# Performance work log

Measured on AMD Instinct MI355X. Metric: run time of the kernel, lower is better.

## Reference

```python
import jax, jax.numpy as jnp
import numpy as np
import math

NUM_HEADS = 8
EMB = 256

def setup_inputs() -> dict:
    key = jax.random.key(0)
    ks = jax.random.split(key, 9)
    B_, N, C = 1024, 64, EMB  # 16 images * 64 windows, 8x8 window, C=256
    nW = 64
    q = jax.random.normal(ks[0], (B_, N, C), dtype=jnp.float32)
    k = jax.random.normal(ks[1], (B_, N, C), dtype=jnp.float32)
    v = jax.random.normal(ks[2], (B_, N, C), dtype=jnp.float32)
    mask = jax.random.normal(ks[3], (nW, N, N), dtype=jnp.float32)
    # MLP params (Linear: y = x @ W^T + b; we store W already transposed for x @ W)
    hid = 4 * C
    s1 = 1.0 / math.sqrt(C)
    s2 = 1.0 / math.sqrt(hid)
    w1 = jax.random.uniform(ks[4], (C, hid), minval=-s1, maxval=s1, dtype=jnp.float32)
    b1 = jax.random.uniform(ks[5], (hid,), minval=-s1, maxval=s1, dtype=jnp.float32)
    w2 = jax.random.uniform(ks[6], (hid, C), minval=-s2, maxval=s2, dtype=jnp.float32)
    b2 = jax.random.uniform(ks[7], (C,), minval=-s2, maxval=s2, dtype=jnp.float32)
    return {"q": q, "k": k, "v": v, "mask": mask, "H": 64, "W": 64,
            "w1": w1, "b1": b1, "w2": w2, "b2": b2}

def reference(q, k, v, mask, H, W, w1, b1, w2, b2):
    B_, N, C = q.shape
    h = NUM_HEADS
    d = C // h
    # separate heads: (B_, h, N, d)
    qh = q.reshape(B_, N, h, d).transpose(0, 2, 1, 3)
    kh = k.reshape(B_, N, h, d).transpose(0, 2, 1, 3)
    vh = v.reshape(B_, N, h, d).transpose(0, 2, 1, 3)
    attn = jnp.einsum('bhnd,bhmd->bhnm', qh, kh)  # raw scores
    nW = mask.shape[0]
    # additive window mask BEFORE scaling (faithful to original order)
    attn = attn.reshape(B_ // nW, nW, h, N, N) + mask[None, :, None, :, :]
    attn = attn.reshape(B_, h, N, N) / math.sqrt(d)
    attn = jax.nn.softmax(attn, axis=-1)
    out = jnp.einsum('bhnm,bhmd->bhnd', attn, vh)
    out = out.transpose(0, 2, 1, 3).reshape(B_, N, C)  # recombine heads
    # linear Mlp (dropout is identity at p=0.0); torch nn.GELU is exact erf
    hmid = jax.nn.gelu(out @ w1 + b1, approximate=False)
    out = out + (hmid @ w2 + b2)
    return out
```

## Files before the change

### kernel.cpp

```cpp
#include <hip/hip_runtime.h>
#include <hip/hip_bf16.h>
#include <cstdint>
#include <cstddef>

typedef __attribute__((ext_vector_type(8))) short bf16x8;
typedef __attribute__((ext_vector_type(4))) float f32x4;

static __device__ __forceinline__ unsigned short f2bf(float f) {
    __hip_bfloat16 h = __float2bfloat16(f);
    return *reinterpret_cast<unsigned short*>(&h);
}

static __device__ __forceinline__ f32x4 mfma_bf16(bf16x8 a, bf16x8 b, f32x4 c) {
    return __builtin_amdgcn_mfma_f32_16x16x32_bf16(a, b, c, 0, 0, 0);
}

static __device__ __forceinline__ bf16x8 pack8(float4 a, float4 b) {
    bf16x8 f;
    f[0]=(short)f2bf(a.x); f[1]=(short)f2bf(a.y); f[2]=(short)f2bf(a.z); f[3]=(short)f2bf(a.w);
    f[4]=(short)f2bf(b.x); f[5]=(short)f2bf(b.y); f[6]=(short)f2bf(b.z); f[7]=(short)f2bf(b.w);
    return f;
}

static __device__ __forceinline__ float gelu_erf(float v) {
    float s = v * 0.70710678118654752f;
    float a = fabsf(s);
    float t = __builtin_amdgcn_rcpf(1.0f + 0.3275911f * a);
    float poly = ((((1.061405429f * t - 1.453152027f) * t + 1.421413741f) * t
                   - 0.284496736f) * t + 0.254829592f) * t;
    float e = 1.0f - poly * __expf(-a * a);
    float erfv = copysignf(e, s);
    return 0.5f * v * (1.0f + erfv);
}

static __device__ __forceinline__ void load_lds16(const unsigned short* g, unsigned short* l) {
    __builtin_amdgcn_global_load_lds(
        (const __attribute__((address_space(1))) unsigned int*)g,
        (__attribute__((address_space(3))) unsigned int*)l, 16, 0, 0);
}

__global__ __launch_bounds__(256) void attn_kernel(
    const float* __restrict__ q, const float* __restrict__ k,
    const float* __restrict__ v, const float* __restrict__ mask,
    float* __restrict__ xout)
{
    __shared__ unsigned short Qs[64][40];
    __shared__ unsigned short Ks[64][40];
    __shared__ unsigned short Vt[32][72];
    __shared__ unsigned short Ps[64][72];

    const int tid  = threadIdx.x;
    const int b    = blockIdx.x >> 3;
    const int h    = blockIdx.x & 7;
    const int lane = tid & 63;
    const int l15  = lane & 15;
    const int g    = lane >> 4;
    const int w    = tid >> 6;

    {
        int row = tid >> 2;
        int seg = tid & 3;
        size_t base = ((size_t)(b * 64 + row)) * 256 + h * 32 + seg * 8;

        float4 a0 = *(const float4*)(q + base);
        float4 a1 = *(const float4*)(q + base + 4);
        unsigned short* p = &Qs[row][seg * 8];
        p[0]=f2bf(a0.x); p[1]=f2bf(a0.y); p[2]=f2bf(a0.z); p[3]=f2bf(a0.w);
        p[4]=f2bf(a1.x); p[5]=f2bf(a1.y); p[6]=f2bf(a1.z); p[7]=f2bf(a1.w);

        a0 = *(const float4*)(k + base);
        a1 = *(const float4*)(k + base + 4);
        p = &Ks[row][seg * 8];
        p[0]=f2bf(a0.x); p[1]=f2bf(a0.y); p[2]=f2bf(a0.z); p[3]=f2bf(a0.w);
        p[4]=f2bf(a1.x); p[5]=f2bf(a1.y); p[6]=f2bf(a1.z); p[7]=f2bf(a1.w);

        a0 = *(const float4*)(v + base);
        a1 = *(const float4*)(v + base + 4);
        int c = seg * 8;
        Vt[c + 0][row] = f2bf(a0.x);
        Vt[c + 1][row] = f2bf(a0.y);
        Vt[c + 2][row] = f2bf(a0.z);
        Vt[c + 3][row] = f2bf(a0.w);
        Vt[c + 4][row] = f2bf(a1.x);
        Vt[c + 5][row] = f2bf(a1.y);
        Vt[c + 6][row] = f2bf(a1.z);
        Vt[c + 7][row] = f2bf(a1.w);
    }
    __syncthreads();

    f32x4 s[4];
    {
        bf16x8 aQ = *(const bf16x8*)&Qs[w * 16 + l15][g * 8];
        #pragma unroll
        for (int ct = 0; ct < 4; ++ct) {
            bf16x8 bK = *(const bf16x8*)&Ks[ct * 16 + l15][g * 8];
            f32x4 z = {0.f, 0.f, 0.f, 0.f};
            s[ct] = mfma_bf16(aQ, bK, z);
        }
    }

    const float* mbase = mask + (size_t)(b & 63) * 4096;
    const float INV = 0.17677669529663688f;
    float rsum[4];
    #pragma unroll
    for (int r = 0; r < 4; ++r) {
        int row = w * 16 + g * 4 + r;
        float pr[4];
        #pragma unroll
        for (int ct = 0; ct < 4; ++ct)
            pr[ct] = (s[ct][r] + mbase[row * 64 + ct * 16 + l15]) * INV;
        float m = fmaxf(fmaxf(pr[0], pr[1]), fmaxf(pr[2], pr[3]));
        #pragma unroll
        for (int off = 1; off < 16; off <<= 1)
            m = fmaxf(m, __shfl_xor(m, off));
        float sum = 0.f;
        #pragma unroll
        for (int ct = 0; ct < 4; ++ct) { pr[ct] = __expf(pr[ct] - m); sum += pr[ct]; }
        #pragma unroll
        for (int off = 1; off < 16; off <<= 1)
            sum += __shfl_xor(sum, off);
        rsum[r] = sum;
        #pragma unroll
        for (int ct = 0; ct < 4; ++ct)
            Ps[row][ct * 16 + l15] = f2bf(pr[ct]);
    }

    f32x4 o[2] = {};
    #pragma unroll
    for (int ks = 0; ks < 2; ++ks) {
        bf16x8 pa = *(const bf16x8*)&Ps[w * 16 + l15][ks * 32 + g * 8];
        #pragma unroll
        for (int n = 0; n < 2; ++n) {
            bf16x8 vb = *(const bf16x8*)&Vt[n * 16 + l15][ks * 32 + g * 8];
            o[n] = mfma_bf16(pa, vb, o[n]);
        }
    }

    #pragma unroll
    for (int n = 0; n < 2; ++n) {
        #pragma unroll
        for (int r = 0; r < 4; ++r) {
            int row = w * 16 + g * 4 + r;
            xout[((size_t)(b * 64 + row)) * 256 + h * 32 + n * 16 + l15] =
                o[n][r] / rsum[r];
        }
    }
}

__global__ __launch_bounds__(256) void prep_w1(const float* __restrict__ src,
                                               unsigned short* __restrict__ dst)
{
    __shared__ float tile[64][65];
    const int kt = blockIdx.x, nb = blockIdx.y;
    const int t = threadIdx.x;
    const int r0 = t >> 4, c4 = (t & 15) * 4;
    #pragma unroll
    for (int p = 0; p < 4; ++p) {
        int kk = r0 + p * 16;
        float4 d = *(const float4*)(src + (size_t)(kt * 64 + kk) * 1024 + nb * 64 + c4);
        tile[kk][c4+0]=d.x; tile[kk][c4+1]=d.y; tile[kk][c4+2]=d.z; tile[kk][c4+3]=d.w;
    }
    __syncthreads();
    #pragma unroll
    for (int i = 0; i < 2; ++i) {
        int f = t + 256 * i;
        int chalf = f >> 8;
        int ksl   = (f >> 7) & 1;
        int nt    = (f >> 6) & 1;
        int gv    = (f >> 4) & 3;
        int l15v  = f & 15;
        int n_local = chalf * 32 + 8 * (l15v >> 2) + 4 * nt + (l15v & 3);
        int k_local = ksl * 32 + gv * 8;
        int c  = nb * 2 + chalf;
        int ks = kt * 2 + ksl;
        unsigned short tmp[8];
        #pragma unroll
        for (int e = 0; e < 8; ++e) tmp[e] = f2bf(tile[k_local + e][n_local]);
        size_t off = (size_t)c * 8192 + (size_t)((ks * 2 + nt) * 512)
                   + (gv * 16 + l15v) * 8;
        *(bf16x8*)(dst + off) = *(const bf16x8*)tmp;
    }
}

__global__ __launch_bounds__(256) void prep_w2(const float* __restrict__ src,
                                               unsigned short* __restrict__ dst)
{
    __shared__ float tile[64][65];
    const int ob = blockIdx.x, kb = blockIdx.y;
    const int t = threadIdx.x;
    const int r0 = t >> 4, c4 = (t & 15) * 4;
    #pragma unroll
    for (int p = 0; p < 4; ++p) {
        int kk = r0 + p * 16;
        float4 d = *(const float4*)(src + (size_t)(kb * 64 + kk) * 256 + ob * 64 + c4);
        tile[kk][c4+0]=d.x; tile[kk][c4+1]=d.y; tile[kk][c4+2]=d.z; tile[kk][c4+3]=d.w;
    }
    __syncthreads();
    #pragma unroll
    for (int i = 0; i < 2; ++i) {
        int f = t + 256 * i;
        int ksl = f >> 8;
        int tq  = (f >> 6) & 3;
        int gv  = (f >> 4) & 3;
        int l15v = f & 15;
        int c_local = tq * 16 + l15v;
        int k_local = ksl * 32 + gv * 8;
        int c = kb * 2 + ksl;
        unsigned short tmp[8];
        #pragma unroll
        for (int e = 0; e < 8; ++e) tmp[e] = f2bf(tile[k_local + e][c_local]);
        size_t off = (size_t)c * 8192 + (size_t)((ob * 4 + tq) * 512)
                   + (gv * 16 + l15v) * 8;
        *(bf16x8*)(dst + off) = *(const bf16x8*)tmp;
    }
}

__global__ __launch_bounds__(512, 4) void mlp_fused(
    const float* __restrict__ xin, float* __restrict__ xio,
    const unsigned short* __restrict__ wt1, const float* __restrict__ b1,
    const unsigned short* __restrict__ wt2, const float* __restrict__ b2)
{
    __shared__ unsigned short w1c[2][8192];
    __shared__ unsigned short w2c[2][8192];
    __shared__ float b1s[1024];

    const int tid  = threadIdx.x;
    const int lane = tid & 63;
    const int l15  = lane & 15;
    const int g    = lane >> 4;
    const int wid  = tid >> 6;
    const int fb   = (g * 16 + l15) * 8;

    const size_t rowbase = (size_t)blockIdx.x * 128;

    auto stage = [&](const unsigned short* gbase, unsigned short* lbase) {
        #pragma unroll
        for (int i = 0; i < 2; ++i) {
            load_lds16(gbase + (i * 512 + tid) * 8,
                       lbase + (i * 512 + wid * 64) * 8);
        }
    };

    stage(wt1, &w1c[0][0]);
    stage(wt2, &w2c[0][0]);

    b1s[tid]       = b1[tid];
    b1s[tid + 512] = b1[tid + 512];

    bf16x8 xf[8];
    {
        const float* xr = xin + (rowbase + wid * 16 + l15) * 256;
        #pragma unroll
        for (int ks = 0; ks < 8; ++ks) {
            float4 a0 = *(const float4*)(xr + ks * 32 + g * 8);
            float4 a1 = *(const float4*)(xr + ks * 32 + g * 8 + 4);
            xf[ks] = pack8(a0, a1);
        }
    }

    f32x4 oacc[16] = {};

    for (int hc = 0; hc < 32; ++hc) {
        const int cur = hc & 1;
        __syncthreads();

        if (hc < 31) {
            stage(wt1 + (size_t)(hc + 1) * 8192, &w1c[cur ^ 1][0]);
            stage(wt2 + (size_t)(hc + 1) * 8192, &w2c[cur ^ 1][0]);
        }

        f32x4 hacc[2] = {};
        #pragma unroll
        for (int ks = 0; ks < 8; ++ks) {
            bf16x8 w0 = *(const bf16x8*)&w1c[cur][(ks * 2 + 0) * 512 + fb];
            bf16x8 w1f = *(const bf16x8*)&w1c[cur][(ks * 2 + 1) * 512 + fb];
            hacc[0] = mfma_bf16(w0,  xf[ks], hacc[0]);
            hacc[1] = mfma_bf16(w1f, xf[ks], hacc[1]);
        }

        const float* bp = &b1s[hc * 32 + g * 8];
        float4 ba = *(const float4*)bp;
        float4 bb = *(const float4*)(bp + 4);
        bf16x8 aH;
        aH[0] = (short)f2bf(gelu_erf(hacc[0][0] + ba.x));
        aH[1] = (short)f2bf(gelu_erf(hacc[0][1] + ba.y));
        aH[2] = (short)f2bf(gelu_erf(hacc[0][2] + ba.z));
        aH[3] = (short)f2bf(gelu_erf(hacc[0][3] + ba.w));
        aH[4] = (short)f2bf(gelu_erf(hacc[1][0] + bb.x));
        aH[5] = (short)f2bf(gelu_erf(hacc[1][1] + bb.y));
        aH[6] = (short)f2bf(gelu_erf(hacc[1][2] + bb.z));
        aH[7] = (short)f2bf(gelu_erf(hacc[1][3] + bb.w));

        #pragma unroll
        for (int n = 0; n < 16; ++n) {
            bf16x8 bF = *(const bf16x8*)&w2c[cur][n * 512 + fb];
            oacc[n] = mfma_bf16(aH, bF, oacc[n]);
        }
    }

    #pragma unroll
    for (int n = 0; n < 16; ++n) {
        int col = n * 16 + l15;
        float bias = b2[col];
        #pragma unroll
        for (int r = 0; r < 4; ++r) {
            size_t idx = (rowbase + wid * 16 + g * 4 + r) * 256 + col;
            xio[idx] = oacc[n][r] + bias + xio[idx];
        }
    }
}

extern "C" void kernel_launch(void* const* d_in, const int* in_sizes, int n_in,
                              void* d_out, int out_size, void* d_ws, size_t ws_size,
                              hipStream_t stream)
{
    const float* q    = (const float*)d_in[0];
    const float* k    = (const float*)d_in[1];
    const float* v    = (const float*)d_in[2];
    const float* mask = (const float*)d_in[3];
    const float* w1   = (const float*)d_in[6];
    const float* b1   = (const float*)d_in[7];
    const float* w2   = (const float*)d_in[8];
    const float* b2   = (const float*)d_in[9];

    float* xio = (float*)d_out;

    unsigned short* wt1 = (unsigned short*)d_ws;
    unsigned short* wt2 = wt1 + (size_t)1024 * 256;

    prep_w1<<<dim3(4, 16), 256, 0, stream>>>(w1, wt1);
    prep_w2<<<dim3(4, 16), 256, 0, stream>>>(w2, wt2);

    attn_kernel<<<8192, 256, 0, stream>>>(q, k, v, mask, xio);

    mlp_fused<<<512, 512, 0, stream>>>(xio, xio, wt1, b1, wt2, b2);
}
```

Baseline: 170.0 us.

## Process two 16-row tiles per wave in fused MLP to halve weight streaming

Each wave now handles 32 rows instead of 16, so every staged W1/W2 chunk in LDS and each LDS fragment read feeds twice as many MFMAs. The grid drops from 512 to 256 blocks, which halves the total global weight traffic and LDS reads per output. In exchange, accumulator registers double (32 f32x4 oacc), launch bounds are relaxed to 2 blocks per CU, and 256 blocks may underfill the device's CUs.

```diff
diff --git a/kernel.cpp b/kernel.cpp
--- a/kernel.cpp
+++ b/kernel.cpp
@@ -215,7 +215,7 @@
     }
 }
 
-__global__ __launch_bounds__(512, 4) void mlp_fused(
+__global__ __launch_bounds__(512, 2) void mlp_fused(
     const float* __restrict__ xin, float* __restrict__ xio,
     const unsigned short* __restrict__ wt1, const float* __restrict__ b1,
     const unsigned short* __restrict__ wt2, const float* __restrict__ b2)
@@ -231,7 +231,7 @@
     const int wid  = tid >> 6;
     const int fb   = (g * 16 + l15) * 8;
 
-    const size_t rowbase = (size_t)blockIdx.x * 128;
+    const size_t rowbase = (size_t)blockIdx.x * 256;
 
     auto stage = [&](const unsigned short* gbase, unsigned short* lbase) {
         #pragma unroll
@@ -247,18 +247,19 @@
     b1s[tid]       = b1[tid];
     b1s[tid + 512] = b1[tid + 512];
 
-    bf16x8 xf[8];
-    {
-        const float* xr = xin + (rowbase + wid * 16 + l15) * 256;
+    bf16x8 xf[2][8];
+    #pragma unroll
+    for (int mt = 0; mt < 2; ++mt) {
+        const float* xr = xin + (rowbase + wid * 32 + mt * 16 + l15) * 256;
         #pragma unroll
         for (int ks = 0; ks < 8; ++ks) {
             float4 a0 = *(const float4*)(xr + ks * 32 + g * 8);
             float4 a1 = *(const float4*)(xr + ks * 32 + g * 8 + 4);
-            xf[ks] = pack8(a0, a1);
-        }
-    }
-
-    f32x4 oacc[16] = {};
+            xf[mt][ks] = pack8(a0, a1);
+        }
+    }
+
+    f32x4 oacc[2][16] = {};
 
     for (int hc = 0; hc < 32; ++hc) {
         const int cur = hc & 1;
@@ -269,43 +270,52 @@
             stage(wt2 + (size_t)(hc + 1) * 8192, &w2c[cur ^ 1][0]);
         }
 
-        f32x4 hacc[2] = {};
+        f32x4 hacc[2][2] = {};
         #pragma unroll
         for (int ks = 0; ks < 8; ++ks) {
-            bf16x8 w0 = *(const bf16x8*)&w1c[cur][(ks * 2 + 0) * 512 + fb];
+            bf16x8 w0  = *(const bf16x8*)&w1c[cur][(ks * 2 + 0) * 512 + fb];
             bf16x8 w1f = *(const bf16x8*)&w1c[cur][(ks * 2 + 1) * 512 + fb];
-            hacc[0] = mfma_bf16(w0,  xf[ks], hacc[0]);
-            hacc[1] = mfma_bf16(w1f, xf[ks], hacc[1]);
+            hacc[0][0] = mfma_bf16(w0,  xf[0][ks], hacc[0][0]);
+            hacc[0][1] = mfma_bf16(w1f, xf[0][ks], hacc[0][1]);
+            hacc[1][0] = mfma_bf16(w0,  xf[1][ks], hacc[1][0]);
+            hacc[1][1] = mfma_bf16(w1f, xf[1][ks], hacc[1][1]);
         }
 
         const float* bp = &b1s[hc * 32 + g * 8];
         float4 ba = *(const float4*)bp;
         float4 bb = *(const float4*)(bp + 4);
-        bf16x8 aH;
-        aH[0] = (short)f2bf(gelu_erf(hacc[0][0] + ba.x));
-        aH[1] = (short)f2bf(gelu_erf(hacc[0][1] + ba.y));
-        aH[2] = (short)f2bf(gelu_erf(hacc[0][2] + ba.z));
-        aH[3] = (short)f2bf(gelu_erf(hacc[0][3] + ba.w));
-        aH[4] = (short)f2bf(gelu_erf(hacc[1][0] + bb.x));
-        aH[5] = (short)f2bf(gelu_erf(hacc[1][1] + bb.y));
-        aH[6] = (short)f2bf(gelu_erf(hacc[1][2] + bb.z));
-        aH[7] = (short)f2bf(gelu_erf(hacc[1][3] + bb.w));
+        bf16x8 aH[2];
+        #pragma unroll
+        for (int mt = 0; mt < 2; ++mt) {
+            aH[mt][0] = (short)f2bf(gelu_erf(hacc[mt][0][0] + ba.x));
+            aH[mt][1] = (short)f2bf(gelu_erf(hacc[mt][0][1] + ba.y));
+            aH[mt][2] = (short)f2bf(gelu_erf(hacc[mt][0][2] + ba.z));
+            aH[mt][3] = (short)f2bf(gelu_erf(hacc[mt][0][3] + ba.w));
+            aH[mt][4] = (short)f2bf(gelu_erf(hacc[mt][1][0] + bb.x));
+            aH[mt][5] = (short)f2bf(gelu_erf(hacc[mt][1][1] + bb.y));
+            aH[mt][6] = (short)f2bf(gelu_erf(hacc[mt][1][2] + bb.z));
+            aH[mt][7] = (short)f2bf(gelu_erf(hacc[mt][1][3] + bb.w));
+        }
 
         #pragma unroll
         for (int n = 0; n < 16; ++n) {
             bf16x8 bF = *(const bf16x8*)&w2c[cur][n * 512 + fb];
-            oacc[n] = mfma_bf16(aH, bF, oacc[n]);
-        }
-    }
-
-    #pragma unroll
-    for (int n = 0; n < 16; ++n) {
-        int col = n * 16 + l15;
-        float bias = b2[col];
-        #pragma unroll
-        for (int r = 0; r < 4; ++r) {
-            size_t idx = (rowbase + wid * 16 + g * 4 + r) * 256 + col;
-            xio[idx] = oacc[n][r] + bias + xio[idx];
+            oacc[0][n] = mfma_bf16(aH[0], bF, oacc[0][n]);
+            oacc[1][n] = mfma_bf16(aH[1], bF, oacc[1][n]);
+        }
+    }
+
+    #pragma unroll
+    for (int mt = 0; mt < 2; ++mt) {
+        #pragma unroll
+        for (int n = 0; n < 16; ++n) {
+            int col = n * 16 + l15;
+            float bias = b2[col];
+            #pragma unroll
+            for (int r = 0; r < 4; ++r) {
+                size_t idx = (rowbase + wid * 32 + mt * 16 + g * 4 + r) * 256 + col;
+                xio[idx] = oacc[mt][n][r] + bias + xio[idx];
+            }
         }
     }
 }
@@ -333,5 +343,5 @@
 
     attn_kernel<<<8192, 256, 0, stream>>>(q, k, v, mask, xio);
 
-    mlp_fused<<<512, 512, 0, stream>>>(xio, xio, wt1, b1, wt2, b2);
-}
+    mlp_fused<<<256, 512, 0, stream>>>(xio, xio, wt1, b1, wt2, b2);
+}
```

Result: slower. 175.2 us (+3.1%).

## Software-pipeline MLP so next chunk's GEMM1+GELU overlaps current GEMM2

Applied to the files above, without the earlier changes.

Restructures the hidden-chunk loop. The first-layer matmul and erf-GELU for chunk i+1 are now computed while the second-layer MFMAs for chunk i run, so the independent VALU work can interleave with matrix instructions. The first-layer weights are prefetched two chunks ahead and the second-layer weights one chunk ahead, using the existing double buffers. The cost is higher register pressure from carrying aH alongside aH_next, plus one redundant first-layer/GELU computation on the final iteration.

```diff
diff --git a/kernel.cpp b/kernel.cpp
--- a/kernel.cpp
+++ b/kernel.cpp
@@ -241,8 +241,9 @@
         }
     };
 
-    stage(wt1, &w1c[0][0]);
-    stage(wt2, &w2c[0][0]);
+    stage(wt1,        &w1c[0][0]);
+    stage(wt2,        &w2c[0][0]);
+    stage(wt1 + 8192, &w1c[1][0]);
 
     b1s[tid]       = b1[tid];
     b1s[tid + 512] = b1[tid + 512];
@@ -260,28 +261,21 @@
 
     f32x4 oacc[16] = {};
 
-    for (int hc = 0; hc < 32; ++hc) {
-        const int cur = hc & 1;
-        __syncthreads();
-
-        if (hc < 31) {
-            stage(wt1 + (size_t)(hc + 1) * 8192, &w1c[cur ^ 1][0]);
-            stage(wt2 + (size_t)(hc + 1) * 8192, &w2c[cur ^ 1][0]);
-        }
-
+    __syncthreads();
+
+    bf16x8 aH;
+    {
         f32x4 hacc[2] = {};
         #pragma unroll
         for (int ks = 0; ks < 8; ++ks) {
-            bf16x8 w0 = *(const bf16x8*)&w1c[cur][(ks * 2 + 0) * 512 + fb];
-            bf16x8 w1f = *(const bf16x8*)&w1c[cur][(ks * 2 + 1) * 512 + fb];
+            bf16x8 w0  = *(const bf16x8*)&w1c[0][(ks * 2 + 0) * 512 + fb];
+            bf16x8 w1f = *(const bf16x8*)&w1c[0][(ks * 2 + 1) * 512 + fb];
             hacc[0] = mfma_bf16(w0,  xf[ks], hacc[0]);
             hacc[1] = mfma_bf16(w1f, xf[ks], hacc[1]);
         }
-
-        const float* bp = &b1s[hc * 32 + g * 8];
+        const float* bp = &b1s[g * 8];
         float4 ba = *(const float4*)bp;
         float4 bb = *(const float4*)(bp + 4);
-        bf16x8 aH;
         aH[0] = (short)f2bf(gelu_erf(hacc[0][0] + ba.x));
         aH[1] = (short)f2bf(gelu_erf(hacc[0][1] + ba.y));
         aH[2] = (short)f2bf(gelu_erf(hacc[0][2] + ba.z));
@@ -290,12 +284,48 @@
         aH[5] = (short)f2bf(gelu_erf(hacc[1][1] + bb.y));
         aH[6] = (short)f2bf(gelu_erf(hacc[1][2] + bb.z));
         aH[7] = (short)f2bf(gelu_erf(hacc[1][3] + bb.w));
-
+    }
+
+    for (int i = 0; i < 32; ++i) {
+        __syncthreads();
+
+        if (i < 31) {
+            stage(wt2 + (size_t)(i + 1) * 8192, &w2c[(i + 1) & 1][0]);
+            if (i < 30)
+                stage(wt1 + (size_t)(i + 2) * 8192, &w1c[i & 1][0]);
+        }
+
+        f32x4 hacc[2] = {};
+        const unsigned short* w1b = &w1c[(i + 1) & 1][0];
+        #pragma unroll
+        for (int ks = 0; ks < 8; ++ks) {
+            bf16x8 w0  = *(const bf16x8*)(w1b + (ks * 2 + 0) * 512 + fb);
+            bf16x8 w1f = *(const bf16x8*)(w1b + (ks * 2 + 1) * 512 + fb);
+            hacc[0] = mfma_bf16(w0,  xf[ks], hacc[0]);
+            hacc[1] = mfma_bf16(w1f, xf[ks], hacc[1]);
+        }
+
+        const float* bp = &b1s[((i + 1) & 31) * 32 + g * 8];
+        float4 ba = *(const float4*)bp;
+        float4 bb = *(const float4*)(bp + 4);
+        bf16x8 aH_next;
+        aH_next[0] = (short)f2bf(gelu_erf(hacc[0][0] + ba.x));
+        aH_next[1] = (short)f2bf(gelu_erf(hacc[0][1] + ba.y));
+        aH_next[2] = (short)f2bf(gelu_erf(hacc[0][2] + ba.z));
+        aH_next[3] = (short)f2bf(gelu_erf(hacc[0][3] + ba.w));
+        aH_next[4] = (short)f2bf(gelu_erf(hacc[1][0] + bb.x));
+        aH_next[5] = (short)f2bf(gelu_erf(hacc[1][1] + bb.y));
+        aH_next[6] = (short)f2bf(gelu_erf(hacc[1][2] + bb.z));
+        aH_next[7] = (short)f2bf(gelu_erf(hacc[1][3] + bb.w));
+
+        const unsigned short* w2b = &w2c[i & 1][0];
         #pragma unroll
         for (int n = 0; n < 16; ++n) {
-            bf16x8 bF = *(const bf16x8*)&w2c[cur][n * 512 + fb];
+            bf16x8 bF = *(const bf16x8*)(w2b + n * 512 + fb);
             oacc[n] = mfma_bf16(aH, bF, oacc[n]);
         }
+
+        aH = aH_next;
     }
 
     #pragma unroll
```

After: 172.6 us. About the same (+1.6%).

## Split MLP hidden chunk across wave pairs with LDS exchange, halve rows per block

Applied to the files above, without the earlier changes.

Restructures the fused MLP kernel so each block handles 64 rows instead of 128, with pairs of waves splitting each 32-wide hidden chunk and the 256-wide output columns. The two halves of the GELU activation are exchanged through a small LDS buffer. Weights are re-laid out into 4096-element halves so the staging buffers shrink, and the grid doubles to 1024 blocks with a higher occupancy hint. This aims for more parallelism, lower per-wave register use and smaller LDS per block. In exchange it adds an extra barrier per chunk, loses the prefetch overlap for W2 (now staged within the same iteration), and re-reads weights twice as often overall.

```diff
diff --git a/kernel.cpp b/kernel.cpp
--- a/kernel.cpp
+++ b/kernel.cpp
@@ -5,6 +5,7 @@
 
 typedef __attribute__((ext_vector_type(8))) short bf16x8;
 typedef __attribute__((ext_vector_type(4))) float f32x4;
+typedef __attribute__((ext_vector_type(4))) unsigned short us4;
 
 static __device__ __forceinline__ unsigned short f2bf(float f) {
     __hip_bfloat16 h = __float2bfloat16(f);
@@ -176,7 +177,7 @@
         unsigned short tmp[8];
         #pragma unroll
         for (int e = 0; e < 8; ++e) tmp[e] = f2bf(tile[k_local + e][n_local]);
-        size_t off = (size_t)c * 8192 + (size_t)((ks * 2 + nt) * 512)
+        size_t off = (size_t)(c * 2 + nt) * 4096 + (size_t)(ks * 512)
                    + (gv * 16 + l15v) * 8;
         *(bf16x8*)(dst + off) = *(const bf16x8*)tmp;
     }
@@ -206,50 +207,50 @@
         int c_local = tq * 16 + l15v;
         int k_local = ksl * 32 + gv * 8;
         int c = kb * 2 + ksl;
+        size_t off = (size_t)(c * 2 + (ob >> 1)) * 4096
+                   + (size_t)((((ob & 1) * 4 + tq)) * 512)
+                   + (gv * 16 + l15v) * 8;
         unsigned short tmp[8];
         #pragma unroll
         for (int e = 0; e < 8; ++e) tmp[e] = f2bf(tile[k_local + e][c_local]);
-        size_t off = (size_t)c * 8192 + (size_t)((ob * 4 + tq) * 512)
-                   + (gv * 16 + l15v) * 8;
         *(bf16x8*)(dst + off) = *(const bf16x8*)tmp;
     }
 }
 
-__global__ __launch_bounds__(512, 4) void mlp_fused(
+__global__ __launch_bounds__(512, 5) void mlp_fused(
     const float* __restrict__ xin, float* __restrict__ xio,
     const unsigned short* __restrict__ wt1, const float* __restrict__ b1,
     const unsigned short* __restrict__ wt2, const float* __restrict__ b2)
 {
-    __shared__ unsigned short w1c[2][8192];
-    __shared__ unsigned short w2c[2][8192];
+    __shared__ unsigned short w1c[2][4096];
+    __shared__ unsigned short w2c[2][4096];
     __shared__ float b1s[1024];
+    __shared__ unsigned short Ex[4][2][256];
 
     const int tid  = threadIdx.x;
     const int lane = tid & 63;
     const int l15  = lane & 15;
     const int g    = lane >> 4;
     const int wid  = tid >> 6;
+    const int p    = wid >> 1;
+    const int nt   = wid & 1;
     const int fb   = (g * 16 + l15) * 8;
 
-    const size_t rowbase = (size_t)blockIdx.x * 128;
-
-    auto stage = [&](const unsigned short* gbase, unsigned short* lbase) {
-        #pragma unroll
-        for (int i = 0; i < 2; ++i) {
-            load_lds16(gbase + (i * 512 + tid) * 8,
-                       lbase + (i * 512 + wid * 64) * 8);
-        }
+    const size_t rowbase = (size_t)blockIdx.x * 64;
+
+    auto stage8k = [&](const unsigned short* gbase, unsigned short* lbase) {
+        load_lds16(gbase + tid * 8, lbase + wid * 512);
     };
 
-    stage(wt1, &w1c[0][0]);
-    stage(wt2, &w2c[0][0]);
+    stage8k(wt1,        &w1c[0][0]);
+    stage8k(wt1 + 4096, &w1c[1][0]);
 
     b1s[tid]       = b1[tid];
     b1s[tid + 512] = b1[tid + 512];
 
     bf16x8 xf[8];
     {
-        const float* xr = xin + (rowbase + wid * 16 + l15) * 256;
+        const float* xr = xin + (rowbase + p * 16 + l15) * 256;
         #pragma unroll
         for (int ks = 0; ks < 8; ++ks) {
             float4 a0 = *(const float4*)(xr + ks * 32 + g * 8);
@@ -258,53 +259,60 @@
         }
     }
 
-    f32x4 oacc[16] = {};
-
-    for (int hc = 0; hc < 32; ++hc) {
-        const int cur = hc & 1;
+    f32x4 oacc[8] = {};
+
+    for (int c = 0; c < 32; ++c) {
         __syncthreads();
 
-        if (hc < 31) {
-            stage(wt1 + (size_t)(hc + 1) * 8192, &w1c[cur ^ 1][0]);
-            stage(wt2 + (size_t)(hc + 1) * 8192, &w2c[cur ^ 1][0]);
-        }
-
-        f32x4 hacc[2] = {};
+        stage8k(wt2 + (size_t)(2 * c + 0) * 4096, &w2c[0][0]);
+        stage8k(wt2 + (size_t)(2 * c + 1) * 4096, &w2c[1][0]);
+
+        f32x4 hacc = {0.f, 0.f, 0.f, 0.f};
         #pragma unroll
         for (int ks = 0; ks < 8; ++ks) {
-            bf16x8 w0 = *(const bf16x8*)&w1c[cur][(ks * 2 + 0) * 512 + fb];
-            bf16x8 w1f = *(const bf16x8*)&w1c[cur][(ks * 2 + 1) * 512 + fb];
-            hacc[0] = mfma_bf16(w0,  xf[ks], hacc[0]);
-            hacc[1] = mfma_bf16(w1f, xf[ks], hacc[1]);
-        }
-
-        const float* bp = &b1s[hc * 32 + g * 8];
-        float4 ba = *(const float4*)bp;
-        float4 bb = *(const float4*)(bp + 4);
+            bf16x8 wf = *(const bf16x8*)&w1c[nt][ks * 512 + fb];
+            hacc = mfma_bf16(wf, xf[ks], hacc);
+        }
+
+        float4 bb = *(const float4*)&b1s[c * 32 + g * 8 + nt * 4];
+        us4 own;
+        own[0] = f2bf(gelu_erf(hacc[0] + bb.x));
+        own[1] = f2bf(gelu_erf(hacc[1] + bb.y));
+        own[2] = f2bf(gelu_erf(hacc[2] + bb.z));
+        own[3] = f2bf(gelu_erf(hacc[3] + bb.w));
+        *(us4*)&Ex[p][nt][lane * 4] = own;
+
+        __syncthreads();
+
+        if (c < 31) {
+            stage8k(wt1 + (size_t)(2 * c + 2) * 4096, &w1c[0][0]);
+            stage8k(wt1 + (size_t)(2 * c + 3) * 4096, &w1c[1][0]);
+        }
+
+        us4 other = *(const us4*)&Ex[p][nt ^ 1][lane * 4];
         bf16x8 aH;
-        aH[0] = (short)f2bf(gelu_erf(hacc[0][0] + ba.x));
-        aH[1] = (short)f2bf(gelu_erf(hacc[0][1] + ba.y));
-        aH[2] = (short)f2bf(gelu_erf(hacc[0][2] + ba.z));
-        aH[3] = (short)f2bf(gelu_erf(hacc[0][3] + ba.w));
-        aH[4] = (short)f2bf(gelu_erf(hacc[1][0] + bb.x));
-        aH[5] = (short)f2bf(gelu_erf(hacc[1][1] + bb.y));
-        aH[6] = (short)f2bf(gelu_erf(hacc[1][2] + bb.z));
-        aH[7] = (short)f2bf(gelu_erf(hacc[1][3] + bb.w));
-
-        #pragma unroll
-        for (int n = 0; n < 16; ++n) {
-            bf16x8 bF = *(const bf16x8*)&w2c[cur][n * 512 + fb];
+        if (nt == 0) {
+            aH[0]=(short)own[0];   aH[1]=(short)own[1];   aH[2]=(short)own[2];   aH[3]=(short)own[3];
+            aH[4]=(short)other[0]; aH[5]=(short)other[1]; aH[6]=(short)other[2]; aH[7]=(short)other[3];
+        } else {
+            aH[0]=(short)other[0]; aH[1]=(short)other[1]; aH[2]=(short)other[2]; aH[3]=(short)other[3];
+            aH[4]=(short)own[0];   aH[5]=(short)own[1];   aH[6]=(short)own[2];   aH[7]=(short)own[3];
+        }
+
+        #pragma unroll
+        for (int n = 0; n < 8; ++n) {
+            bf16x8 bF = *(const bf16x8*)&w2c[nt][n * 512 + fb];
             oacc[n] = mfma_bf16(aH, bF, oacc[n]);
         }
     }
 
     #pragma unroll
-    for (int n = 0; n < 16; ++n) {
-        int col = n * 16 + l15;
+    for (int n = 0; n < 8; ++n) {
+        int col = nt * 128 + n * 16 + l15;
         float bias = b2[col];
         #pragma unroll
         for (int r = 0; r < 4; ++r) {
-            size_t idx = (rowbase + wid * 16 + g * 4 + r) * 256 + col;
+            size_t idx = (rowbase + p * 16 + g * 4 + r) * 256 + col;
             xio[idx] = oacc[n][r] + bias + xio[idx];
         }
     }
@@ -333,5 +341,5 @@
 
     attn_kernel<<<8192, 256, 0, stream>>>(q, k, v, mask, xio);
 
-    mlp_fused<<<512, 512, 0, stream>>>(xio, xio, wt1, b1, wt2, b2);
-}
+    mlp_fused<<<1024, 512, 0, stream>>>(xio, xio, wt1, b1, wt2, b2);
+}
```

After: 181.3 us. 6.6% more time.
